# Performance work log

Hardware: AMD Instinct MI355X
Metric: run time of the kernel (lower is better)

The kernel has to match this reference:

```python
import jax, jax.numpy as jnp
import numpy as np

B, N, C_IN = 8, 4096, 64
M, K = 1024, 32          # npoints, knn k
C_COV, C_OUT = 64, 128   # mlp_cov out channels, mlp_f out channels


def setup_inputs() -> dict:
    key = jax.random.key(0)
    k0, k1, k2, k3 = jax.random.split(key, 4)
    return {
        "f": jax.random.normal(k0, (B, C_IN, N), jnp.float32),
        "xyz": jax.random.normal(k1, (B, N, 3), jnp.float32),
        "W_cov": jax.random.normal(k2, (C_COV, 9), jnp.float32) * 0.1,
        "b_cov": jnp.zeros((C_COV,), jnp.float32),
        "W_f": jax.random.normal(k3, (C_OUT, C_IN + C_COV), jnp.float32) * 0.1,
        "b_f": jnp.zeros((C_OUT,), jnp.float32),
    }


def _fps_single(pts):
    """Farthest point sampling on one cloud [N,3] -> [M] indices (start at 0)."""
    n = pts.shape[0]

    def step(carry, _):
        dists, far = carry
        d = jnp.sum((pts - pts[far]) ** 2, axis=-1)   # [N]
        dists = jnp.minimum(dists, d)
        nxt = jnp.argmax(dists).astype(jnp.int32)
        return (dists, nxt), far

    init = (jnp.full((n,), 1e10, pts.dtype), jnp.int32(0))
    _, idxs = jax.lax.scan(step, init, None, length=M)
    return idxs  # [M]


def reference(f, xyz, W_cov, b_cov, W_f, b_f):
    # FPS: [B, M] sampled indices, gather new centroids [B, M, 3]
    sample_idx = jax.vmap(_fps_single)(xyz)
    xyz_new = jnp.take_along_axis(xyz, sample_idx[:, :, None], axis=1)  # [B,M,3]

    # Brute-force KNN: squared distances [B, M, N], take k smallest
    d2 = jnp.sum((xyz_new[:, :, None, :] - xyz[:, None, :, :]) ** 2, axis=-1)
    _, idx = jax.lax.top_k(-d2, K)  # idx: [B, M, K]

    # Group features [B, C, M, K] and max-pool over neighbors -> [B, C, M]
    grouped = jax.vmap(lambda fb, ib: fb[:, ib])(f, idx)
    f_max = grouped.max(axis=-1)

    # Local covariance of neighbor coordinates -> [B, 9, M]
    nbr = jax.vmap(lambda pb, ib: pb[ib])(xyz, idx)          # [B, M, K, 3]
    centered = nbr - nbr.mean(axis=2, keepdims=True)
    covm = jnp.einsum('bmki,bmkj->bmij', centered, centered) / K  # [B,M,3,3]
    cov9 = covm.reshape(B, M, 9).transpose(0, 2, 1)          # [B, 9, M]

    # mlp_cov: 1x1 conv (9 -> C_COV) + ReLU
    f_cov = jax.nn.relu(jnp.einsum('co,bom->bcm', W_cov, cov9) + b_cov[None, :, None])

    # concat on channel dim, mlp_f: 1x1 conv (C_IN+C_COV -> C_OUT) + ReLU
    f_cat = jnp.concatenate([f_max, f_cov], axis=1)          # [B, 128, M]
    out = jax.nn.relu(jnp.einsum('co,bom->bcm', W_f, f_cat) + b_f[None, :, None])
    return (out, xyz_new)
```

## Files before the change

### kernel.cpp

```cpp
#include <hip/hip_runtime.h>
#include <hip/hip_bf16.h>
#include <stdint.h>

#define BATCH 8
#define NPTS  4096
#define CIN   64
#define MPTS  1024
#define KNN   32
#define CCOV  64
#define COUT  128
#define CCAP  1024

typedef unsigned long long u64;
typedef unsigned int u32;

__global__ void k_transpose(const float* __restrict__ f, float* __restrict__ fT) {
    __shared__ float tile[64][65];
    int b  = blockIdx.y;
    int n0 = blockIdx.x * 64;
    int tx = threadIdx.x & 63;
    int ty = threadIdx.x >> 6;
#pragma unroll
    for (int r = 0; r < 16; ++r) {
        int c = r * 4 + ty;
        tile[c][tx] = f[((size_t)b * CIN + c) * NPTS + n0 + tx];
    }
    __syncthreads();
#pragma unroll
    for (int r = 0; r < 16; ++r) {
        int n = r * 4 + ty;
        fT[((size_t)b * NPTS + n0 + n) * CIN + tx] = tile[tx][n];
    }
}

template <int CTRL>
__device__ __forceinline__ float dpp_step_max(float x) {
    int xi = __float_as_int(x);
    int yi = __builtin_amdgcn_update_dpp(xi, xi, CTRL, 0xF, 0xF, false);
    return fmaxf(x, __int_as_float(yi));
}
__device__ __forceinline__ float wave_max_dpp(float x) {
    x = dpp_step_max<0x111>(x);
    x = dpp_step_max<0x112>(x);
    x = dpp_step_max<0x114>(x);
    x = dpp_step_max<0x118>(x);
    x = dpp_step_max<0x142>(x);
    x = dpp_step_max<0x143>(x);
    return __int_as_float(__builtin_amdgcn_readlane(__float_as_int(x), 63));
}

__launch_bounds__(512, 1)
__global__ void k_fps(const float* __restrict__ xyz, float* __restrict__ xyz_new) {
    __shared__ float sx[NPTS], sy[NPTS], sz[NPTS];
    __shared__ int   sel[MPTS];
    __shared__ __align__(16) float wmax[2][8];
    __shared__ u64 wkey[2], wkey2[2];
    __shared__ int wcnt[2];
    __shared__ int cand[2][32];

    int b    = blockIdx.x;
    int tid  = threadIdx.x;
    int lane = tid & 63, wid = tid >> 6;
    const float* xb = xyz + (size_t)b * NPTS * 3;
    float px[8], py[8], pz[8], dist[8];
#pragma unroll
    for (int j = 0; j < 8; ++j) {
        int i = tid + 512 * j;
        px[j] = xb[i * 3 + 0];
        py[j] = xb[i * 3 + 1];
        pz[j] = xb[i * 3 + 2];
        sx[i] = px[j]; sy[i] = py[j]; sz[i] = pz[j];
        dist[j] = 1e30f;
    }
    __syncthreads();

    int far = 0;
    float* xout = xyz_new + (size_t)b * MPTS * 3;

    for (int m = 0; m < MPTS; ++m) {
        int p = m & 1;
        float fx = sx[far], fy = sy[far], fz = sz[far];
        if (tid == 0) {
            xout[m * 3 + 0] = fx;
            xout[m * 3 + 1] = fy;
            xout[m * 3 + 2] = fz;
            sel[m] = far;
            wcnt[p] = 0; wkey[p] = 0; wkey2[p] = 0;
        }
        float lmax = 0.f;
#pragma unroll
        for (int j = 0; j < 8; ++j) {
            float dx = px[j] - fx, dy = py[j] - fy, dz = pz[j] - fz;
            float d  = fmaf(dx, dx, fmaf(dy, dy, dz * dz));
            dist[j] = fminf(dist[j], d);
            lmax = fmaxf(lmax, dist[j]);
        }
        float wm = wave_max_dpp(lmax);
        if (lane == 0) wmax[p][wid] = wm;
        __syncthreads();

        float4 a4 = *(const float4*)&wmax[p][0];
        float4 b4 = *(const float4*)&wmax[p][4];
        float gmax = fmaxf(fmaxf(fmaxf(a4.x, a4.y), fmaxf(a4.z, a4.w)),
                           fmaxf(fmaxf(b4.x, b4.y), fmaxf(b4.z, b4.w)));
        float thresh = gmax * (1.0f - 4e-6f);

        bool any = false;
#pragma unroll
        for (int j = 0; j < 8; ++j) any |= (dist[j] >= thresh);
        if (any) {
#pragma unroll
            for (int j = 0; j < 8; ++j) {
                if (dist[j] >= thresh) {
                    int i = tid + 512 * j;
                    int pos = atomicAdd(&wcnt[p], 1);
                    if (pos < 32) cand[p][pos] = i;
                    atomicMax(&wkey[p],
                              ((u64)__float_as_uint(dist[j]) << 32) | (u32)(~(u32)i));
                }
            }
        }
        __syncthreads();

        int nc = wcnt[p];
        if (nc == 1) {
            far = (int)(~(u32)wkey[p]);
        } else {
            int nc2 = nc < 32 ? nc : 32;
            for (int c = wid; c < nc2; c += 8) {
                int i = cand[p][c];
                double cx = (double)sx[i], cy = (double)sy[i], cz = (double)sz[i];
                double dmin = 1e10;
                for (int t = lane; t <= m; t += 64) {
                    int s = sel[t];
                    double ddx = __dsub_rn(cx, (double)sx[s]);
                    double ddy = __dsub_rn(cy, (double)sy[s]);
                    double ddz = __dsub_rn(cz, (double)sz[s]);
                    double d64 = __dadd_rn(__dadd_rn(__dmul_rn(ddx, ddx),
                                                     __dmul_rn(ddy, ddy)),
                                           __dmul_rn(ddz, ddz));
                    dmin = fmin(dmin, d64);
                }
#pragma unroll
                for (int off = 32; off; off >>= 1)
                    dmin = fmin(dmin, __shfl_xor(dmin, off));
                if (lane == 0)
                    atomicMax(&wkey2[p],
                              ((u64)__double_as_longlong(dmin) & ~0xFFFull) |
                              (u64)((~(u32)i) & 0xFFFu));
            }
            __syncthreads();
            far = (int)((~(u32)wkey2[p]) & 0xFFFu);
        }
    }
}

__launch_bounds__(64)
__global__ void k_knn(const float* __restrict__ xyz, const float* __restrict__ xyz_new,
                      const float* __restrict__ fT, const float* __restrict__ Wcov,
                      const float* __restrict__ bcov, float* __restrict__ fcat) {
    __shared__ u32 cidx[CCAP];
    __shared__ u64 kbuf[CCAP];
    __shared__ int sknn[KNN];
    __shared__ int cnt;

    int q = blockIdx.x;
    int b = q >> 10, m = q & 1023;
    int lane = threadIdx.x;
    const float* xb = xyz + (size_t)b * NPTS * 3;

    float cxf = xyz_new[((size_t)b * MPTS + m) * 3 + 0];
    float cyf = xyz_new[((size_t)b * MPTS + m) * 3 + 1];
    float czf = xyz_new[((size_t)b * MPTS + m) * 3 + 2];
    double cx = (double)cxf, cy = (double)cyf, cz = (double)czf;

    if (lane == 0) cnt = 0;

    float d[64];
    float lmin = 1e30f;
#pragma unroll
    for (int t = 0; t < 64; ++t) {
        int i = lane + 64 * t;
        float dx = cxf - xb[i * 3 + 0];
        float dy = cyf - xb[i * 3 + 1];
        float dz = czf - xb[i * 3 + 2];
        d[t] = fmaf(dx, dx, fmaf(dy, dy, dz * dz));
        lmin = fminf(lmin, d[t]);
    }
    float c0  = wave_max_dpp(lmin);
    float cut = c0 * (1.0f + 4e-6f);
    __syncthreads();

#pragma unroll
    for (int t = 0; t < 64; ++t) {
        if (d[t] <= cut) {
            int pos = atomicAdd(&cnt, 1);
            if (pos < CCAP) cidx[pos] = (u32)(lane + 64 * t);
        }
    }
    __syncthreads();
    int n0 = cnt;

    if (n0 <= CCAP) {
        for (int c = lane; c < n0; c += 64) {
            int i = (int)cidx[c];
            double dx = __dsub_rn(cx, (double)xb[i * 3 + 0]);
            double dy = __dsub_rn(cy, (double)xb[i * 3 + 1]);
            double dz = __dsub_rn(cz, (double)xb[i * 3 + 2]);
            double d2 = __dadd_rn(__dadd_rn(__dmul_rn(dx, dx), __dmul_rn(dy, dy)),
                                  __dmul_rn(dz, dz));
            kbuf[c] = ((u64)__double_as_longlong(d2) & ~0xFFFull) | (u64)i;
        }
        u64 thr = 0;
        for (int it = 0; it < KNN; ++it) {
            u64 best = ~0ull;
            for (int c = lane; c < n0; c += 64) {
                u64 v = kbuf[c];
                if (v >= thr && v < best) best = v;
            }
#pragma unroll
            for (int off = 1; off < 64; off <<= 1) {
                u64 o = __shfl_xor(best, off);
                if (o < best) best = o;
            }
            if (lane == 0) sknn[it] = (int)(best & 0xFFFull);
            thr = best + 1;
        }
    } else {
        u64 thr = 0;
        for (int it = 0; it < KNN; ++it) {
            u64 best = ~0ull;
#pragma unroll 4
            for (int t = 0; t < 64; ++t) {
                int i = lane + 64 * t;
                double dx = __dsub_rn(cx, (double)xb[i * 3 + 0]);
                double dy = __dsub_rn(cy, (double)xb[i * 3 + 1]);
                double dz = __dsub_rn(cz, (double)xb[i * 3 + 2]);
                double d2 = __dadd_rn(__dadd_rn(__dmul_rn(dx, dx), __dmul_rn(dy, dy)),
                                      __dmul_rn(dz, dz));
                u64 v = ((u64)__double_as_longlong(d2) & ~0xFFFull) | (u64)i;
                if (v >= thr && v < best) best = v;
            }
#pragma unroll
            for (int off = 1; off < 64; off <<= 1) {
                u64 o = __shfl_xor(best, off);
                if (o < best) best = o;
            }
            if (lane == 0) sknn[it] = (int)(best & 0xFFFull);
            thr = best + 1;
        }
    }
    __syncthreads();

    int nk = sknn[lane & 31];
    float nx = xb[nk * 3 + 0], ny = xb[nk * 3 + 1], nz = xb[nk * 3 + 2];
    float sxs = nx, sys = ny, szs = nz;
#pragma unroll
    for (int off = 1; off < 64; off <<= 1) {
        sxs += __shfl_xor(sxs, off);
        sys += __shfl_xor(sys, off);
        szs += __shfl_xor(szs, off);
    }
    float mx = sxs * (1.f / 64.f), my = sys * (1.f / 64.f), mz = szs * (1.f / 64.f);
    float ux = nx - mx, uy = ny - my, uz = nz - mz;
    float pxx = ux * ux, pxy = ux * uy, pxz = ux * uz;
    float pyy = uy * uy, pyz = uy * uz, pzz = uz * uz;
#pragma unroll
    for (int off = 1; off < 64; off <<= 1) {
        pxx += __shfl_xor(pxx, off);
        pxy += __shfl_xor(pxy, off);
        pxz += __shfl_xor(pxz, off);
        pyy += __shfl_xor(pyy, off);
        pyz += __shfl_xor(pyz, off);
        pzz += __shfl_xor(pzz, off);
    }
    const float inv = 1.f / 64.f;
    float c9[9];
    c9[0] = pxx * inv; c9[1] = pxy * inv; c9[2] = pxz * inv;
    c9[3] = pxy * inv; c9[4] = pyy * inv; c9[5] = pyz * inv;
    c9[6] = pxz * inv; c9[7] = pyz * inv; c9[8] = pzz * inv;

    float acc = bcov[lane];
#pragma unroll
    for (int j = 0; j < 9; ++j) acc = fmaf(Wcov[lane * 9 + j], c9[j], acc);
    float fcov = fmaxf(acc, 0.f);

    float fm = -1e30f;
#pragma unroll
    for (int kk = 0; kk < KNN; ++kk) {
        int ni = sknn[kk];
        fm = fmaxf(fm, fT[((size_t)b * NPTS + ni) * CIN + lane]);
    }

    float* dst = fcat + (size_t)q * (CIN + CCOV);
    dst[lane]       = fm;
    dst[CIN + lane] = fcov;
}

__global__ void k_mlp(const float* __restrict__ fcat, const float* __restrict__ Wf,
                      const float* __restrict__ bf, float* __restrict__ out) {
    __shared__ float tile[32][132];
    int b  = blockIdx.y;
    int m0 = blockIdx.x * 32;
    int tid = threadIdx.x;
    const float4* src = (const float4*)(fcat + ((size_t)b * MPTS + m0) * 128);
#pragma unroll
    for (int r = 0; r < 4; ++r) {
        int e  = tid + 256 * r;
        int mm = e >> 5;
        int c4 = e & 31;
        float4 v = src[e];
        *(float4*)&tile[mm][c4 * 4] = v;
    }
    __syncthreads();

    int m   = tid & 31;
    int cog = tid >> 5;
    float acc[16];
#pragma unroll
    for (int j = 0; j < 16; ++j) acc[j] = bf[cog * 16 + j];

    for (int c4 = 0; c4 < 32; ++c4) {
        float4 fv = *(const float4*)&tile[m][c4 * 4];
#pragma unroll
        for (int j = 0; j < 16; ++j) {
            int co = cog * 16 + j;
            float4 wv = ((const float4*)(Wf + (size_t)co * 128))[c4];
            acc[j] = fmaf(wv.x, fv.x, acc[j]);
            acc[j] = fmaf(wv.y, fv.y, acc[j]);
            acc[j] = fmaf(wv.z, fv.z, acc[j]);
            acc[j] = fmaf(wv.w, fv.w, acc[j]);
        }
    }
#pragma unroll
    for (int j = 0; j < 16; ++j) {
        int co = cog * 16 + j;
        out[((size_t)b * COUT + co) * MPTS + m0 + m] = fmaxf(acc[j], 0.f);
    }
}

extern "C" void kernel_launch(void* const* d_in, const int* in_sizes, int n_in,
                              void* d_out, int out_size, void* d_ws, size_t ws_size,
                              hipStream_t stream) {
    const float* f    = (const float*)d_in[0];
    const float* xyz  = (const float*)d_in[1];
    const float* Wcov = (const float*)d_in[2];
    const float* bcov = (const float*)d_in[3];
    const float* Wf   = (const float*)d_in[4];
    const float* bf   = (const float*)d_in[5];

    float* out     = (float*)d_out;
    float* xyz_new = out + (size_t)BATCH * COUT * MPTS;

    float* fT   = (float*)d_ws;
    float* fcat = fT + (size_t)BATCH * NPTS * CIN;

    k_transpose<<<dim3(64, BATCH), 256, 0, stream>>>(f, fT);
    k_fps<<<BATCH, 512, 0, stream>>>(xyz, xyz_new);
    k_knn<<<BATCH * MPTS, 64, 0, stream>>>(xyz, xyz_new, fT, Wcov, bcov, fcat);
    k_mlp<<<dim3(MPTS / 32, BATCH), 256, 0, stream>>>(fcat, Wf, bf, out);
}
```

Before: 1.148 ms.

## Use per-wave ballot keys to remove second barrier in FPS argmax

Each wave now packs its max distance, a near-tie candidate count from ballots, and a candidate index into one 64-bit key. After a single barrier, all threads reduce the eight keys and, when exactly one candidate lies within the threshold, take the index without any atomics or a second barrier. The per-iteration global writes of sampled coordinates are replaced by one bulk write after the loop. The atomic/refinement path is kept for ties, but the per-wave threshold differs slightly from the global one, which could change tie handling in edge cases.

```diff
diff --git a/kernel.cpp b/kernel.cpp
--- a/kernel.cpp
+++ b/kernel.cpp
@@ -53,10 +53,10 @@
 __global__ void k_fps(const float* __restrict__ xyz, float* __restrict__ xyz_new) {
     __shared__ float sx[NPTS], sy[NPTS], sz[NPTS];
     __shared__ int   sel[MPTS];
-    __shared__ __align__(16) float wmax[2][8];
-    __shared__ u64 wkey[2], wkey2[2];
-    __shared__ int wcnt[2];
-    __shared__ int cand[2][32];
+    __shared__ __align__(16) u64 wkeys[2][8];
+    __shared__ u64 wkey2[2];
+    __shared__ int rcnt[2];
+    __shared__ int rcand[2][32];
 
     int b    = blockIdx.x;
     int tid  = threadIdx.x;
@@ -75,17 +75,13 @@
     __syncthreads();
 
     int far = 0;
-    float* xout = xyz_new + (size_t)b * MPTS * 3;
 
     for (int m = 0; m < MPTS; ++m) {
         int p = m & 1;
         float fx = sx[far], fy = sy[far], fz = sz[far];
         if (tid == 0) {
-            xout[m * 3 + 0] = fx;
-            xout[m * 3 + 1] = fy;
-            xout[m * 3 + 2] = fz;
             sel[m] = far;
-            wcnt[p] = 0; wkey[p] = 0; wkey2[p] = 0;
+            rcnt[p] = 0; wkey2[p] = 0;
         }
         float lmax = 0.f;
 #pragma unroll
@@ -96,39 +92,57 @@
             lmax = fmaxf(lmax, dist[j]);
         }
         float wm = wave_max_dpp(lmax);
-        if (lane == 0) wmax[p][wid] = wm;
+        float wthresh = wm * (1.0f - 4e-6f);
+        int cw = 0;
+        u32 idxw = 0xFFFu;
+#pragma unroll
+        for (int j = 0; j < 8; ++j) {
+            u64 bj = __ballot(dist[j] >= wthresh);
+            cw += (int)__popcll(bj);
+            if (bj) idxw = (u32)(wid * 64 + (int)__builtin_ctzll(bj) + 512 * j);
+        }
+        u64 key = ((u64)__float_as_uint(wm) << 32) |
+                  ((u64)(u32)(cw > 255 ? 255 : cw) << 12) | (u64)idxw;
+        if (lane == 0) wkeys[p][wid] = key;
         __syncthreads();
 
-        float4 a4 = *(const float4*)&wmax[p][0];
-        float4 b4 = *(const float4*)&wmax[p][4];
-        float gmax = fmaxf(fmaxf(fmaxf(a4.x, a4.y), fmaxf(a4.z, a4.w)),
-                           fmaxf(fmaxf(b4.x, b4.y), fmaxf(b4.z, b4.w)));
-        float thresh = gmax * (1.0f - 4e-6f);
-
-        bool any = false;
-#pragma unroll
-        for (int j = 0; j < 8; ++j) any |= (dist[j] >= thresh);
-        if (any) {
+        ulonglong2 q0 = *(const ulonglong2*)&wkeys[p][0];
+        ulonglong2 q1 = *(const ulonglong2*)&wkeys[p][2];
+        ulonglong2 q2 = *(const ulonglong2*)&wkeys[p][4];
+        ulonglong2 q3 = *(const ulonglong2*)&wkeys[p][6];
+        u64 ka = q0.x > q0.y ? q0.x : q0.y;
+        u64 kb = q1.x > q1.y ? q1.x : q1.y;
+        u64 kc = q2.x > q2.y ? q2.x : q2.y;
+        u64 kd = q3.x > q3.y ? q3.x : q3.y;
+        u64 ke = ka > kb ? ka : kb;
+        u64 kf = kc > kd ? kc : kd;
+        u64 kmax = ke > kf ? ke : kf;
+        float gmax = __uint_as_float((u32)(kmax >> 32));
+        float gthresh = gmax * (1.0f - 4e-6f);
+        int tot = 0;
+        {
+            u64 ks[8] = {q0.x, q0.y, q1.x, q1.y, q2.x, q2.y, q3.x, q3.y};
+#pragma unroll
+            for (int w = 0; w < 8; ++w) {
+                float wmw = __uint_as_float((u32)(ks[w] >> 32));
+                if (wmw >= gthresh) tot += (int)((ks[w] >> 12) & 0xFFull);
+            }
+        }
+
+        if (tot == 1) {
+            far = (int)(kmax & 0xFFFull);
+        } else {
 #pragma unroll
             for (int j = 0; j < 8; ++j) {
-                if (dist[j] >= thresh) {
-                    int i = tid + 512 * j;
-                    int pos = atomicAdd(&wcnt[p], 1);
-                    if (pos < 32) cand[p][pos] = i;
-                    atomicMax(&wkey[p],
-                              ((u64)__float_as_uint(dist[j]) << 32) | (u32)(~(u32)i));
+                if (dist[j] >= gthresh) {
+                    int pos = atomicAdd(&rcnt[p], 1);
+                    if (pos < 32) rcand[p][pos] = tid + 512 * j;
                 }
             }
-        }
-        __syncthreads();
-
-        int nc = wcnt[p];
-        if (nc == 1) {
-            far = (int)(~(u32)wkey[p]);
-        } else {
-            int nc2 = nc < 32 ? nc : 32;
-            for (int c = wid; c < nc2; c += 8) {
-                int i = cand[p][c];
+            __syncthreads();
+            int nc = rcnt[p] < 32 ? rcnt[p] : 32;
+            for (int c = wid; c < nc; c += 8) {
+                int i = rcand[p][c];
                 double cx = (double)sx[i], cy = (double)sy[i], cz = (double)sz[i];
                 double dmin = 1e10;
                 for (int t = lane; t <= m; t += 64) {
@@ -152,6 +166,15 @@
             __syncthreads();
             far = (int)((~(u32)wkey2[p]) & 0xFFFu);
         }
+    }
+
+    __syncthreads();
+    float* xout = xyz_new + (size_t)b * MPTS * 3;
+    for (int mm = tid; mm < MPTS; mm += 512) {
+        int s = sel[mm];
+        xout[mm * 3 + 0] = sx[s];
+        xout[mm * 3 + 1] = sy[s];
+        xout[mm * 3 + 2] = sz[s];
     }
 }
 
```

Result: slower. 1.180 ms (+2.8%).
